# Kernel tuning notes

Measured on AMD Instinct MI355X. Metric: run time of the kernel, lower is better.

Reference implementation:

```python
import math
import jax, jax.numpy as jnp
import numpy as np

N_HEADS = 16

def setup_inputs() -> dict:
    key = jax.random.key(0)
    k1, k2, k3 = jax.random.split(key, 3)
    B, T, C = 2, 2048, 1024
    x = jax.random.normal(k1, (B, T, C), dtype=jnp.float32)
    # Linear weights stored as [in, out] so y = x @ W + b (same math as torch Linear)
    w_qkv = jax.random.normal(k2, (C, 3 * C), dtype=jnp.float32) * (1.0 / math.sqrt(C))
    b_qkv = jnp.zeros((3 * C,), dtype=jnp.float32)
    w_out = jax.random.normal(k3, (C, C), dtype=jnp.float32) * (1.0 / math.sqrt(C))
    b_out = jnp.zeros((C,), dtype=jnp.float32)
    return {"x": x, "w_qkv": w_qkv, "b_qkv": b_qkv, "w_out": w_out, "b_out": b_out}

def reference(x, w_qkv, b_qkv, w_out, b_out):
    B, T, C = x.shape
    H = N_HEADS
    hd = C // H
    qkv = (x @ w_qkv + b_qkv).reshape(B, T, 3, H, hd)
    q, k, v = qkv[:, :, 0], qkv[:, :, 1], qkv[:, :, 2]  # [B,T,H,hd]
    scale = 1.0 / math.sqrt(hd)
    att = jnp.einsum('bqhd,bkhd->bhqk', q, k) * scale  # [B,H,T,T]
    causal = jnp.tril(jnp.ones((T, T), dtype=bool))
    att = jnp.where(causal[None, None], att, jnp.float32(-jnp.inf))
    att = jax.nn.softmax(att, axis=-1)
    # dropout p=0.0 -> identity (eval mode)
    y = jnp.einsum('bhqk,bkhd->bqhd', att, v).reshape(B, T, C)
    return y @ w_out + b_out
```

## Files before the change

kernel.cpp:

```cpp
#include <hip/hip_runtime.h>
#include <hip/hip_bf16.h>
#include <stdint.h>


typedef __bf16 bf16_t;
typedef __attribute__((ext_vector_type(8))) __bf16 bf16x8;
typedef __attribute__((ext_vector_type(4))) __bf16 bf16x4;
typedef __attribute__((ext_vector_type(4))) short short4v;
typedef __attribute__((ext_vector_type(4))) float f32x4;

static_assert(sizeof(bf16x8) == 16, "bf16x8 must be 16B");

#if defined(__has_builtin)
#if __has_builtin(__builtin_amdgcn_mfma_f32_16x16x16bf16_1k)
#define HAVE_MFMA16 1
#endif
#if __has_builtin(__builtin_amdgcn_exp2f)
#define EXP2F(x) __builtin_amdgcn_exp2f(x)
#endif
#endif
#ifndef HAVE_MFMA16
#define HAVE_MFMA16 0
#endif
#ifndef EXP2F
#define EXP2F(x) exp2f(x)
#endif

__device__ inline void async_copy16(const bf16_t* gsrc, bf16_t* lds_dst) {
  __builtin_amdgcn_global_load_lds(
      (const __attribute__((address_space(1))) uint32_t*)(const void*)gsrc,
      (__attribute__((address_space(3))) uint32_t*)(void*)lds_dst,
      16, 0, 0);
}

__global__ __launch_bounds__(256) void prep_kernel(
    const float* __restrict__ x, const float* __restrict__ wq,
    const float* __restrict__ wo, bf16_t* __restrict__ xb,
    bf16_t* __restrict__ wqkvT, bf16_t* __restrict__ woutT) {
  __shared__ bf16_t tile[32][33];
  const int bid = blockIdx.x;
  if (bid < 2048) {
    const int i = bid * 256 + threadIdx.x;
    const float4* s = (const float4*)x;
    float4 a = s[i * 2], b = s[i * 2 + 1];
    bf16x8 o;
    o[0] = (bf16_t)a.x; o[1] = (bf16_t)a.y; o[2] = (bf16_t)a.z; o[3] = (bf16_t)a.w;
    o[4] = (bf16_t)b.x; o[5] = (bf16_t)b.y; o[6] = (bf16_t)b.z; o[7] = (bf16_t)b.w;
    ((bf16x8*)xb)[i] = o;
    return;
  }
  const bool isq = bid < 5120;
  const int id = isq ? bid - 2048 : bid - 5120;
  const int C = isq ? 3072 : 1024;
  const int R = 1024;
  const int nbx = isq ? 96 : 32;
  const float* in = isq ? wq : wo;
  bf16_t* out = isq ? wqkvT : woutT;
  const int c0 = (id % nbx) * 32, r0 = (id / nbx) * 32;
  const int tx = threadIdx.x & 31;
  const int ty = threadIdx.x >> 5;
#pragma unroll
  for (int i = 0; i < 4; i++) {
    int r = ty + i * 8;
    tile[r][tx] = (bf16_t)in[(size_t)(r0 + r) * C + c0 + tx];
  }
  __syncthreads();
#pragma unroll
  for (int i = 0; i < 4; i++) {
    int r = ty + i * 8;
    out[(size_t)(c0 + r) * R + r0 + tx] = tile[tx][r];
  }
}

template <bool OUT_F32>
__global__ __launch_bounds__(256) void gemm_bt_kernel(
    const bf16_t* __restrict__ A, const bf16_t* __restrict__ Bt,
    const float* __restrict__ bias, void* __restrict__ Cv, int M, int N,
    int K) {
  __shared__ __align__(16) bf16_t sA[128 * 32];
  __shared__ __align__(16) bf16_t sB[128 * 32];
  const int tid = threadIdx.x;
  const int wave = tid >> 6, lane = tid & 63;
  const int quad = lane >> 4, l16 = lane & 15;
  const int wm = (wave >> 1) * 64, wn = (wave & 1) * 64;
  const int bm = blockIdx.y * 128, bn = blockIdx.x * 128;

  const int srow = wave * 16 + (lane >> 2);
  const int skk = (lane & 3) * 8;
  const bf16_t* gA = A + (size_t)(bm + srow) * K + skk;
  const bf16_t* gB = Bt + (size_t)(bn + srow) * K + skk;
  bf16_t* lA = sA + wave * 512;
  bf16_t* lB = sB + wave * 512;

  f32x4 acc[4][4] = {};

  for (int k0 = 0; k0 < K; k0 += 32) {
    __syncthreads();
    async_copy16(gA + k0, lA);
    async_copy16(gA + (size_t)64 * K + k0, lA + 2048);
    async_copy16(gB + k0, lB);
    async_copy16(gB + (size_t)64 * K + k0, lB + 2048);
    __syncthreads();

    bf16x8 af[4], bfr[4];
#pragma unroll
    for (int i = 0; i < 4; i++)
      af[i] = *(const bf16x8*)&sA[(wm + i * 16 + l16) * 32 + quad * 8];
#pragma unroll
    for (int j = 0; j < 4; j++)
      bfr[j] = *(const bf16x8*)&sB[(wn + j * 16 + l16) * 32 + quad * 8];
#pragma unroll
    for (int i = 0; i < 4; i++)
#pragma unroll
      for (int j = 0; j < 4; j++)
        acc[i][j] = __builtin_amdgcn_mfma_f32_16x16x32_bf16(af[i], bfr[j],
                                                            acc[i][j], 0, 0, 0);
  }

#pragma unroll
  for (int j = 0; j < 4; j++) {
    const int col = bn + wn + j * 16 + l16;
    const float bv = bias[col];
#pragma unroll
    for (int i = 0; i < 4; i++) {
#pragma unroll
      for (int r = 0; r < 4; r++) {
        const int row = bm + wm + i * 16 + quad * 4 + r;
        const float v = acc[i][j][r] + bv;
        if (OUT_F32)
          ((float*)Cv)[(size_t)row * N + col] = v;
        else
          ((bf16_t*)Cv)[(size_t)row * N + col] = (bf16_t)v;
      }
    }
  }
}

#if HAVE_MFMA16
__global__ __launch_bounds__(256, 4) void attn_kernel(
    const bf16_t* __restrict__ qkv, bf16_t* __restrict__ Y) {
  constexpr int T = 2048, C3 = 3072;
  constexpr float CSC = 0.18033688f;
  constexpr float MB = 20.0f;
  __shared__ __align__(16) bf16_t sK[2][64 * 64];
  __shared__ __align__(16) bf16_t sVt[2][64 * 64];

  const int tid = threadIdx.x;
  const int wave = tid >> 6, lane = tid & 63;
  const int quad = lane >> 4, l16 = lane & 15;
  const int bh = blockIdx.y;
  const int flip = (bh >> 3) & 1;
  const int vv = ((int)blockIdx.x + ((bh >> 4) & 1) * 8) & 31;
  const int X = flip ? (31 - vv) : vv;
  const int q0 = X * 64;
  const int b = bh >> 4, h = bh & 15;
  const size_t base = (size_t)b * T * C3 + (size_t)h * 64;

  const int qrow = q0 + wave * 16 + l16;
  const bf16x8 qf0 = *(const bf16x8*)&qkv[base + (size_t)qrow * C3 + quad * 8];
  const bf16x8 qf1 =
      *(const bf16x8*)&qkv[base + (size_t)qrow * C3 + 32 + quad * 8];

  f32x4 o[4] = {};
  float l_acc = 0.f;

  const int t = tid >> 2, seg = tid & 3;
  const bf16_t* gK = &qkv[base + (size_t)t * C3 + 1024 + seg * 16];
  const int kq = tid >> 4, dq = tid & 15;
  const bf16_t* gV = &qkv[base + (size_t)(4 * kq) * C3 + 2048 + dq * 4];

  const int ktiles = X + 1;

  bf16x8 kr0 = *(const bf16x8*)gK;
  bf16x8 kr1 = *(const bf16x8*)(gK + 8);
  bf16x4 vA0 = *(const bf16x4*)gV;
  bf16x4 vA1 = *(const bf16x4*)(gV + C3);
  bf16x4 vA2 = *(const bf16x4*)(gV + 2 * C3);
  bf16x4 vA3 = *(const bf16x4*)(gV + 3 * C3);

  for (int kt = 0; kt < ktiles; kt++) {
    const int p = kt & 1;
    *(bf16x8*)&sK[p][t * 64 + (((2 * seg + 0) ^ (t & 7)) << 3)] = kr0;
    *(bf16x8*)&sK[p][t * 64 + (((2 * seg + 1) ^ (t & 7)) << 3)] = kr1;
#pragma unroll
    for (int i = 0; i < 4; i++) {
      const int d = dq * 4 + i;
      bf16x4 w;
      w[0] = vA0[i]; w[1] = vA1[i]; w[2] = vA2[i]; w[3] = vA3[i];
      *(bf16x4*)&sVt[p][d * 64 + ((kq ^ (d & 15)) << 2)] = w;
    }
    if (kt + 1 < ktiles) {
      const size_t off = (size_t)(kt + 1) * 64 * C3;
      kr0 = *(const bf16x8*)(gK + off);
      kr1 = *(const bf16x8*)(gK + off + 8);
      vA0 = *(const bf16x4*)(gV + off);
      vA1 = *(const bf16x4*)(gV + off + C3);
      vA2 = *(const bf16x4*)(gV + off + 2 * C3);
      vA3 = *(const bf16x4*)(gV + off + 3 * C3);
    }
    __syncthreads();

    const bool last = (kt == ktiles - 1);
    const int jmax = last ? wave : 3;
#pragma unroll
    for (int j = 0; j < 4; j++) {
      if (j > jmax) continue;
      const int trow = j * 16 + l16;
      bf16x8 kf0 = *(const bf16x8*)&sK[p][trow * 64 + ((quad ^ (trow & 7)) << 3)];
      bf16x8 kf1 =
          *(const bf16x8*)&sK[p][trow * 64 + (((4 + quad) ^ (trow & 7)) << 3)];
      f32x4 s2 = {};
      __builtin_amdgcn_s_setprio(1);
      s2 = __builtin_amdgcn_mfma_f32_16x16x32_bf16(kf0, qf0, s2, 0, 0, 0);
      s2 = __builtin_amdgcn_mfma_f32_16x16x32_bf16(kf1, qf1, s2, 0, 0, 0);
      __builtin_amdgcn_s_setprio(0);
      const bool diag = last && (j == wave);
#pragma unroll
      for (int r = 0; r < 4; r++) {
        float pv = EXP2F(fmaf(s2[r], CSC, -MB));
        if (diag && (quad * 4 + r > l16)) pv = 0.f;
        s2[r] = pv;
        l_acc += pv;
      }
      bf16x4 pb;
      pb[0] = (bf16_t)s2[0]; pb[1] = (bf16_t)s2[1];
      pb[2] = (bf16_t)s2[2]; pb[3] = (bf16_t)s2[3];
      union { bf16x4 b; short4v s; } u;
      u.b = pb;
      const short4v pa = u.s;
      __builtin_amdgcn_s_setprio(1);
#pragma unroll
      for (int n16 = 0; n16 < 4; n16++) {
        const int d = n16 * 16 + l16;
        const short4v vf = *(const short4v*)&sVt[p][d * 64 +
                                                    (((j * 4 + quad) ^ (d & 15))
                                                     << 2)];
        o[n16] =
            __builtin_amdgcn_mfma_f32_16x16x16bf16_1k(pa, vf, o[n16], 0, 0, 0);
      }
      __builtin_amdgcn_s_setprio(0);
    }
  }

  l_acc += __shfl_xor(l_acc, 16);
  l_acc += __shfl_xor(l_acc, 32);
#pragma unroll
  for (int r = 0; r < 4; r++) {
    const float lr = __shfl(l_acc, quad * 4 + r);
    const float inv = 1.0f / lr;
    const int row = q0 + wave * 16 + quad * 4 + r;
#pragma unroll
    for (int n16 = 0; n16 < 4; n16++)
      Y[((size_t)b * T + row) * 1024 + h * 64 + n16 * 16 + l16] =
          (bf16_t)(o[n16][r] * inv);
  }
}
#else
__global__ __launch_bounds__(256, 4) void attn_kernel(
    const bf16_t* __restrict__ qkv, bf16_t* __restrict__ Y) {
  constexpr int T = 2048, C3 = 3072;
  constexpr float CSC = 0.18033688f;
  constexpr float MB = 20.0f;
  __shared__ __align__(16) bf16_t sK[64 * 64];
  __shared__ __align__(16) bf16_t sVt[64 * 64];
  __shared__ __align__(16) bf16_t sP[4][16 * 64];

  const int tid = threadIdx.x;
  const int wave = tid >> 6, lane = tid & 63;
  const int quad = lane >> 4, l16 = lane & 15;
  const int bh = blockIdx.y;
  const int flip = (bh >> 3) & 1;
  const int vv = ((int)blockIdx.x + ((bh >> 4) & 1) * 8) & 31;
  const int X = flip ? (31 - vv) : vv;
  const int q0 = X * 64;
  const int b = bh >> 4, h = bh & 15;
  const size_t base = (size_t)b * T * C3 + (size_t)h * 64;

  const int qrow = q0 + wave * 16 + l16;
  const bf16x8 qf0 = *(const bf16x8*)&qkv[base + (size_t)qrow * C3 + quad * 8];
  const bf16x8 qf1 =
      *(const bf16x8*)&qkv[base + (size_t)qrow * C3 + 32 + quad * 8];

  f32x4 o[4] = {};
  float l_i[4] = {0.f, 0.f, 0.f, 0.f};

  const int t = tid >> 2, seg = tid & 3;
  const int tk = t & 7, tg3 = t >> 3;
  const bf16_t* gK = &qkv[base + (size_t)t * C3 + 1024 + seg * 16];
  const bf16_t* gV = &qkv[base + (size_t)t * C3 + 2048 + seg * 16];

  const int ktiles = X + 1;

  bf16x8 kr0 = *(const bf16x8*)gK;
  bf16x8 kr1 = *(const bf16x8*)(gK + 8);
  bf16x8 vr0 = *(const bf16x8*)gV;
  bf16x8 vr1 = *(const bf16x8*)(gV + 8);

  for (int kt = 0; kt < ktiles; kt++) {
    __syncthreads();
    *(bf16x8*)&sK[t * 64 + (((2 * seg + 0) ^ tk) << 3)] = kr0;
    *(bf16x8*)&sK[t * 64 + (((2 * seg + 1) ^ tk) << 3)] = kr1;
#pragma unroll
    for (int i = 0; i < 8; i++) {
      const int d = seg * 16 + i;
      sVt[d * 64 + ((tg3 ^ (d >> 3)) << 3) + (t & 7)] = vr0[i];
    }
#pragma unroll
    for (int i = 0; i < 8; i++) {
      const int d = seg * 16 + 8 + i;
      sVt[d * 64 + ((tg3 ^ (d >> 3)) << 3) + (t & 7)] = vr1[i];
    }
    __syncthreads();

    if (kt + 1 < ktiles) {
      const size_t off = (size_t)(kt + 1) * 64 * C3;
      kr0 = *(const bf16x8*)(gK + off);
      kr1 = *(const bf16x8*)(gK + off + 8);
      vr0 = *(const bf16x8*)(gV + off);
      vr1 = *(const bf16x8*)(gV + off + 8);
    }

    f32x4 s[4] = {};
#pragma unroll
    for (int j = 0; j < 4; j++) {
      const int kkey = l16 & 7;
      bf16x8 kf0 =
          *(const bf16x8*)&sK[(j * 16 + l16) * 64 + ((quad ^ kkey) << 3)];
      bf16x8 kf1 =
          *(const bf16x8*)&sK[(j * 16 + l16) * 64 + (((4 + quad) ^ kkey) << 3)];
      s[j] = __builtin_amdgcn_mfma_f32_16x16x32_bf16(qf0, kf0, s[j], 0, 0, 0);
      s[j] = __builtin_amdgcn_mfma_f32_16x16x32_bf16(qf1, kf1, s[j], 0, 0, 0);
    }

#pragma unroll
    for (int j = 0; j < 4; j++)
#pragma unroll
      for (int r = 0; r < 4; r++) s[j][r] = EXP2F(fmaf(s[j][r], CSC, -MB));
    if (kt == ktiles - 1) {
      const int k0 = kt * 64;
#pragma unroll
      for (int j = 0; j < 4; j++) {
        const int kcol = k0 + j * 16 + l16;
#pragma unroll
        for (int r = 0; r < 4; r++)
          if (kcol > q0 + wave * 16 + quad * 4 + r) s[j][r] = 0.f;
      }
    }
#pragma unroll
    for (int j = 0; j < 4; j++)
#pragma unroll
      for (int r = 0; r < 4; r++) l_i[r] += s[j][r];

    bf16_t* sp = &sP[wave][0];
#pragma unroll
    for (int j = 0; j < 4; j++)
#pragma unroll
      for (int r = 0; r < 4; r++) {
        const int m = quad * 4 + r;
        const int kw = (m + (m >> 3)) & 7;
        sp[m * 64 + ((((2 * j + (l16 >> 3)) ^ kw)) << 3) + (l16 & 7)] =
            (bf16_t)s[j][r];
      }

    const int kap = (l16 + (l16 >> 3)) & 7;
#pragma unroll
    for (int s2 = 0; s2 < 2; s2++) {
      bf16x8 pf =
          *(const bf16x8*)&sp[l16 * 64 + (((4 * s2 + quad) ^ kap) << 3)];
#pragma unroll
      for (int j = 0; j < 4; j++) {
        const int d = j * 16 + l16;
        bf16x8 vf =
            *(const bf16x8*)&sVt[d * 64 + (((4 * s2 + quad) ^ (d >> 3)) << 3)];
        o[j] = __builtin_amdgcn_mfma_f32_16x16x32_bf16(pf, vf, o[j], 0, 0, 0);
      }
    }
  }

#pragma unroll
  for (int r = 0; r < 4; r++) {
    float l = l_i[r];
#pragma unroll
    for (int off = 1; off < 16; off <<= 1) l += __shfl_xor(l, off);
    const float inv = 1.0f / l;
    const int row = q0 + wave * 16 + quad * 4 + r;
#pragma unroll
    for (int j = 0; j < 4; j++)
      Y[((size_t)b * T + row) * 1024 + h * 64 + j * 16 + l16] =
          (bf16_t)(o[j][r] * inv);
  }
}
#endif

extern "C" void kernel_launch(void* const* d_in, const int* in_sizes, int n_in,
                              void* d_out, int out_size, void* d_ws,
                              size_t ws_size, hipStream_t stream) {
  const float* x = nullptr;
  const float* w_qkv = nullptr;
  const float* b_qkv = nullptr;
  const float* w_out = nullptr;
  const float* b_out = nullptr;
  for (int i = 0; i < n_in; i++) {
    switch (in_sizes[i]) {
      case 4194304: x = (const float*)d_in[i]; break;
      case 3145728: w_qkv = (const float*)d_in[i]; break;
      case 3072:    b_qkv = (const float*)d_in[i]; break;
      case 1048576: w_out = (const float*)d_in[i]; break;
      case 1024:    b_out = (const float*)d_in[i]; break;
      default: break;
    }
  }
  float* out = (float*)d_out;

  bf16_t* xb = (bf16_t*)d_ws;
  bf16_t* wqkvT = xb + (size_t)4194304;
  bf16_t* woutT = wqkvT + (size_t)3145728;
  bf16_t* qkv = woutT + (size_t)1048576;
  bf16_t* Y = qkv + (size_t)12582912;

  prep_kernel<<<6144, 256, 0, stream>>>(x, w_qkv, w_out, xb, wqkvT, woutT);
  gemm_bt_kernel<false><<<dim3(24, 32), 256, 0, stream>>>(
      xb, wqkvT, b_qkv, (void*)qkv, 4096, 3072, 1024);
  attn_kernel<<<dim3(32, 32), 256, 0, stream>>>(qkv, Y);
  gemm_bt_kernel<true><<<dim3(8, 32), 256, 0, stream>>>(
      Y, woutT, b_out, (void*)out, 4096, 1024, 1024);
}
```

Before: 190.8 us.

## Pair causal query tiles per attention block for balanced work

Each attention block now processes two query tiles, X and 31-X, one after the other, so every block does the same total number of key tiles. The grid is halved to 16x32 blocks. This replaces the previous flip/rotate scheduling heuristic and aims to remove tail imbalance from the triangular causal workload. In exchange there are fewer blocks (512) to fill the GPU, and the two halves of each block run serially, with the first K/V tile of the second pass prefetched during the last iteration of the first.

New measurement: 195.5 us. 1.03x slower.

```diff
diff --git a/kernel.cpp b/kernel.cpp
--- a/kernel.cpp
+++ b/kernel.cpp
@@ -149,27 +149,13 @@
   const int wave = tid >> 6, lane = tid & 63;
   const int quad = lane >> 4, l16 = lane & 15;
   const int bh = blockIdx.y;
-  const int flip = (bh >> 3) & 1;
-  const int vv = ((int)blockIdx.x + ((bh >> 4) & 1) * 8) & 31;
-  const int X = flip ? (31 - vv) : vv;
-  const int q0 = X * 64;
   const int b = bh >> 4, h = bh & 15;
   const size_t base = (size_t)b * T * C3 + (size_t)h * 64;
-
-  const int qrow = q0 + wave * 16 + l16;
-  const bf16x8 qf0 = *(const bf16x8*)&qkv[base + (size_t)qrow * C3 + quad * 8];
-  const bf16x8 qf1 =
-      *(const bf16x8*)&qkv[base + (size_t)qrow * C3 + 32 + quad * 8];
-
-  f32x4 o[4] = {};
-  float l_acc = 0.f;
 
   const int t = tid >> 2, seg = tid & 3;
   const bf16_t* gK = &qkv[base + (size_t)t * C3 + 1024 + seg * 16];
   const int kq = tid >> 4, dq = tid & 15;
   const bf16_t* gV = &qkv[base + (size_t)(4 * kq) * C3 + 2048 + dq * 4];
-
-  const int ktiles = X + 1;
 
   bf16x8 kr0 = *(const bf16x8*)gK;
   bf16x8 kr1 = *(const bf16x8*)(gK + 8);
@@ -178,81 +164,101 @@
   bf16x4 vA2 = *(const bf16x4*)(gV + 2 * C3);
   bf16x4 vA3 = *(const bf16x4*)(gV + 3 * C3);
 
-  for (int kt = 0; kt < ktiles; kt++) {
-    const int p = kt & 1;
-    *(bf16x8*)&sK[p][t * 64 + (((2 * seg + 0) ^ (t & 7)) << 3)] = kr0;
-    *(bf16x8*)&sK[p][t * 64 + (((2 * seg + 1) ^ (t & 7)) << 3)] = kr1;
-#pragma unroll
-    for (int i = 0; i < 4; i++) {
-      const int d = dq * 4 + i;
-      bf16x4 w;
-      w[0] = vA0[i]; w[1] = vA1[i]; w[2] = vA2[i]; w[3] = vA3[i];
-      *(bf16x4*)&sVt[p][d * 64 + ((kq ^ (d & 15)) << 2)] = w;
-    }
-    if (kt + 1 < ktiles) {
-      const size_t off = (size_t)(kt + 1) * 64 * C3;
-      kr0 = *(const bf16x8*)(gK + off);
-      kr1 = *(const bf16x8*)(gK + off + 8);
-      vA0 = *(const bf16x4*)(gV + off);
-      vA1 = *(const bf16x4*)(gV + off + C3);
-      vA2 = *(const bf16x4*)(gV + off + 2 * C3);
-      vA3 = *(const bf16x4*)(gV + off + 3 * C3);
-    }
-    __syncthreads();
-
-    const bool last = (kt == ktiles - 1);
-    const int jmax = last ? wave : 3;
-#pragma unroll
-    for (int j = 0; j < 4; j++) {
-      if (j > jmax) continue;
-      const int trow = j * 16 + l16;
-      bf16x8 kf0 = *(const bf16x8*)&sK[p][trow * 64 + ((quad ^ (trow & 7)) << 3)];
-      bf16x8 kf1 =
-          *(const bf16x8*)&sK[p][trow * 64 + (((4 + quad) ^ (trow & 7)) << 3)];
-      f32x4 s2 = {};
-      __builtin_amdgcn_s_setprio(1);
-      s2 = __builtin_amdgcn_mfma_f32_16x16x32_bf16(kf0, qf0, s2, 0, 0, 0);
-      s2 = __builtin_amdgcn_mfma_f32_16x16x32_bf16(kf1, qf1, s2, 0, 0, 0);
-      __builtin_amdgcn_s_setprio(0);
-      const bool diag = last && (j == wave);
-#pragma unroll
-      for (int r = 0; r < 4; r++) {
-        float pv = EXP2F(fmaf(s2[r], CSC, -MB));
-        if (diag && (quad * 4 + r > l16)) pv = 0.f;
-        s2[r] = pv;
-        l_acc += pv;
-      }
-      bf16x4 pb;
-      pb[0] = (bf16_t)s2[0]; pb[1] = (bf16_t)s2[1];
-      pb[2] = (bf16_t)s2[2]; pb[3] = (bf16_t)s2[3];
-      union { bf16x4 b; short4v s; } u;
-      u.b = pb;
-      const short4v pa = u.s;
-      __builtin_amdgcn_s_setprio(1);
-#pragma unroll
-      for (int n16 = 0; n16 < 4; n16++) {
-        const int d = n16 * 16 + l16;
-        const short4v vf = *(const short4v*)&sVt[p][d * 64 +
-                                                    (((j * 4 + quad) ^ (d & 15))
-                                                     << 2)];
-        o[n16] =
-            __builtin_amdgcn_mfma_f32_16x16x16bf16_1k(pa, vf, o[n16], 0, 0, 0);
-      }
-      __builtin_amdgcn_s_setprio(0);
-    }
-  }
-
-  l_acc += __shfl_xor(l_acc, 16);
-  l_acc += __shfl_xor(l_acc, 32);
-#pragma unroll
-  for (int r = 0; r < 4; r++) {
-    const float lr = __shfl(l_acc, quad * 4 + r);
-    const float inv = 1.0f / lr;
-    const int row = q0 + wave * 16 + quad * 4 + r;
-#pragma unroll
-    for (int n16 = 0; n16 < 4; n16++)
-      Y[((size_t)b * T + row) * 1024 + h * 64 + n16 * 16 + l16] =
-          (bf16_t)(o[n16][r] * inv);
+#pragma unroll 1
+  for (int qs = 0; qs < 2; qs++) {
+    const int X = qs ? (31 - (int)blockIdx.x) : (int)blockIdx.x;
+    const int q0 = X * 64;
+    const int qrow = q0 + wave * 16 + l16;
+    const bf16x8 qf0 =
+        *(const bf16x8*)&qkv[base + (size_t)qrow * C3 + quad * 8];
+    const bf16x8 qf1 =
+        *(const bf16x8*)&qkv[base + (size_t)qrow * C3 + 32 + quad * 8];
+
+    f32x4 o[4] = {};
+    float l_acc = 0.f;
+    const int ktiles = X + 1;
+
+    if (qs) __syncthreads();
+
+    for (int kt = 0; kt < ktiles; kt++) {
+      const int p = kt & 1;
+      *(bf16x8*)&sK[p][t * 64 + (((2 * seg + 0) ^ (t & 7)) << 3)] = kr0;
+      *(bf16x8*)&sK[p][t * 64 + (((2 * seg + 1) ^ (t & 7)) << 3)] = kr1;
+#pragma unroll
+      for (int i = 0; i < 4; i++) {
+        const int d = dq * 4 + i;
+        bf16x4 w;
+        w[0] = vA0[i]; w[1] = vA1[i]; w[2] = vA2[i]; w[3] = vA3[i];
+        *(bf16x4*)&sVt[p][d * 64 + ((kq ^ (d & 15)) << 2)] = w;
+      }
+      const int nkt = (kt + 1 < ktiles) ? (kt + 1) : (qs ? -1 : 0);
+      if (nkt >= 0) {
+        const size_t off = (size_t)nkt * 64 * C3;
+        kr0 = *(const bf16x8*)(gK + off);
+        kr1 = *(const bf16x8*)(gK + off + 8);
+        vA0 = *(const bf16x4*)(gV + off);
+        vA1 = *(const bf16x4*)(gV + off + C3);
+        vA2 = *(const bf16x4*)(gV + off + 2 * C3);
+        vA3 = *(const bf16x4*)(gV + off + 3 * C3);
+      }
+      __syncthreads();
+
+      const bool last = (kt == ktiles - 1);
+      const int jmax = last ? wave : 3;
+#pragma unroll
+      for (int j = 0; j < 4; j++) {
+        if (j > jmax) continue;
+        const int trow = j * 16 + l16;
+        bf16x8 kf0 =
+            *(const bf16x8*)&sK[p][trow * 64 + ((quad ^ (trow & 7)) << 3)];
+        bf16x8 kf1 =
+            *(const bf16x8*)&sK[p][trow * 64 + (((4 + quad) ^ (trow & 7)) << 3)];
+        f32x4 s2 = {};
+        __builtin_amdgcn_s_setprio(1);
+        s2 = __builtin_amdgcn_mfma_f32_16x16x32_bf16(kf0, qf0, s2, 0, 0, 0);
+        s2 = __builtin_amdgcn_mfma_f32_16x16x32_bf16(kf1, qf1, s2, 0, 0, 0);
+        __builtin_amdgcn_s_setprio(0);
+        const bool diag = last && (j == wave);
+#pragma unroll
+        for (int r = 0; r < 4; r++) {
+          float pv = EXP2F(fmaf(s2[r], CSC, -MB));
+          if (diag && (quad * 4 + r > l16)) pv = 0.f;
+          s2[r] = pv;
+          l_acc += pv;
+        }
+        bf16x4 pb;
+        pb[0] = (bf16_t)s2[0]; pb[1] = (bf16_t)s2[1];
+        pb[2] = (bf16_t)s2[2]; pb[3] = (bf16_t)s2[3];
+        union { bf16x4 bv; short4v sv; } u;
+        u.bv = pb;
+        const short4v pa = u.sv;
+        __builtin_amdgcn_s_setprio(1);
+#pragma unroll
+        for (int n16 = 0; n16 < 4; n16++) {
+          const int d = n16 * 16 + l16;
+          const short4v vf = *(const short4v*)&sVt[p][d * 64 +
+                                                      (((j * 4 + quad) ^
+                                                        (d & 15))
+                                                       << 2)];
+          o[n16] = __builtin_amdgcn_mfma_f32_16x16x16bf16_1k(pa, vf, o[n16],
+                                                             0, 0, 0);
+        }
+        __builtin_amdgcn_s_setprio(0);
+      }
+    }
+
+    l_acc += __shfl_xor(l_acc, 16);
+    l_acc += __shfl_xor(l_acc, 32);
+#pragma unroll
+    for (int r = 0; r < 4; r++) {
+      const float lr = __shfl(l_acc, quad * 4 + r);
+      const float inv = 1.0f / lr;
+      const int row = q0 + wave * 16 + quad * 4 + r;
+#pragma unroll
+      for (int n16 = 0; n16 < 4; n16++)
+        Y[((size_t)b * T + row) * 1024 + h * 64 + n16 * 16 + l16] =
+            (bf16_t)(o[n16][r] * inv);
+    }
   }
 }
 #else
@@ -269,125 +275,128 @@
   const int wave = tid >> 6, lane = tid & 63;
   const int quad = lane >> 4, l16 = lane & 15;
   const int bh = blockIdx.y;
-  const int flip = (bh >> 3) & 1;
-  const int vv = ((int)blockIdx.x + ((bh >> 4) & 1) * 8) & 31;
-  const int X = flip ? (31 - vv) : vv;
-  const int q0 = X * 64;
   const int b = bh >> 4, h = bh & 15;
   const size_t base = (size_t)b * T * C3 + (size_t)h * 64;
-
-  const int qrow = q0 + wave * 16 + l16;
-  const bf16x8 qf0 = *(const bf16x8*)&qkv[base + (size_t)qrow * C3 + quad * 8];
-  const bf16x8 qf1 =
-      *(const bf16x8*)&qkv[base + (size_t)qrow * C3 + 32 + quad * 8];
-
-  f32x4 o[4] = {};
-  float l_i[4] = {0.f, 0.f, 0.f, 0.f};
 
   const int t = tid >> 2, seg = tid & 3;
   const int tk = t & 7, tg3 = t >> 3;
   const bf16_t* gK = &qkv[base + (size_t)t * C3 + 1024 + seg * 16];
   const bf16_t* gV = &qkv[base + (size_t)t * C3 + 2048 + seg * 16];
 
-  const int ktiles = X + 1;
-
-  bf16x8 kr0 = *(const bf16x8*)gK;
-  bf16x8 kr1 = *(const bf16x8*)(gK + 8);
-  bf16x8 vr0 = *(const bf16x8*)gV;
-  bf16x8 vr1 = *(const bf16x8*)(gV + 8);
-
-  for (int kt = 0; kt < ktiles; kt++) {
-    __syncthreads();
-    *(bf16x8*)&sK[t * 64 + (((2 * seg + 0) ^ tk) << 3)] = kr0;
-    *(bf16x8*)&sK[t * 64 + (((2 * seg + 1) ^ tk) << 3)] = kr1;
-#pragma unroll
-    for (int i = 0; i < 8; i++) {
-      const int d = seg * 16 + i;
-      sVt[d * 64 + ((tg3 ^ (d >> 3)) << 3) + (t & 7)] = vr0[i];
-    }
-#pragma unroll
-    for (int i = 0; i < 8; i++) {
-      const int d = seg * 16 + 8 + i;
-      sVt[d * 64 + ((tg3 ^ (d >> 3)) << 3) + (t & 7)] = vr1[i];
-    }
-    __syncthreads();
-
-    if (kt + 1 < ktiles) {
-      const size_t off = (size_t)(kt + 1) * 64 * C3;
-      kr0 = *(const bf16x8*)(gK + off);
-      kr1 = *(const bf16x8*)(gK + off + 8);
-      vr0 = *(const bf16x8*)(gV + off);
-      vr1 = *(const bf16x8*)(gV + off + 8);
-    }
-
-    f32x4 s[4] = {};
-#pragma unroll
-    for (int j = 0; j < 4; j++) {
-      const int kkey = l16 & 7;
-      bf16x8 kf0 =
-          *(const bf16x8*)&sK[(j * 16 + l16) * 64 + ((quad ^ kkey) << 3)];
-      bf16x8 kf1 =
-          *(const bf16x8*)&sK[(j * 16 + l16) * 64 + (((4 + quad) ^ kkey) << 3)];
-      s[j] = __builtin_amdgcn_mfma_f32_16x16x32_bf16(qf0, kf0, s[j], 0, 0, 0);
-      s[j] = __builtin_amdgcn_mfma_f32_16x16x32_bf16(qf1, kf1, s[j], 0, 0, 0);
-    }
-
-#pragma unroll
-    for (int j = 0; j < 4; j++)
-#pragma unroll
-      for (int r = 0; r < 4; r++) s[j][r] = EXP2F(fmaf(s[j][r], CSC, -MB));
-    if (kt == ktiles - 1) {
-      const int k0 = kt * 64;
+#pragma unroll 1
+  for (int qs = 0; qs < 2; qs++) {
+    const int X = qs ? (31 - (int)blockIdx.x) : (int)blockIdx.x;
+    const int q0 = X * 64;
+    const int qrow = q0 + wave * 16 + l16;
+    const bf16x8 qf0 =
+        *(const bf16x8*)&qkv[base + (size_t)qrow * C3 + quad * 8];
+    const bf16x8 qf1 =
+        *(const bf16x8*)&qkv[base + (size_t)qrow * C3 + 32 + quad * 8];
+
+    f32x4 o[4] = {};
+    float l_i[4] = {0.f, 0.f, 0.f, 0.f};
+    const int ktiles = X + 1;
+
+    bf16x8 kr0 = *(const bf16x8*)gK;
+    bf16x8 kr1 = *(const bf16x8*)(gK + 8);
+    bf16x8 vr0 = *(const bf16x8*)gV;
+    bf16x8 vr1 = *(const bf16x8*)(gV + 8);
+
+    for (int kt = 0; kt < ktiles; kt++) {
+      __syncthreads();
+      *(bf16x8*)&sK[t * 64 + (((2 * seg + 0) ^ tk) << 3)] = kr0;
+      *(bf16x8*)&sK[t * 64 + (((2 * seg + 1) ^ tk) << 3)] = kr1;
+#pragma unroll
+      for (int i = 0; i < 8; i++) {
+        const int d = seg * 16 + i;
+        sVt[d * 64 + ((tg3 ^ (d >> 3)) << 3) + (t & 7)] = vr0[i];
+      }
+#pragma unroll
+      for (int i = 0; i < 8; i++) {
+        const int d = seg * 16 + 8 + i;
+        sVt[d * 64 + ((tg3 ^ (d >> 3)) << 3) + (t & 7)] = vr1[i];
+      }
+      __syncthreads();
+
+      if (kt + 1 < ktiles) {
+        const size_t off = (size_t)(kt + 1) * 64 * C3;
+        kr0 = *(const bf16x8*)(gK + off);
+        kr1 = *(const bf16x8*)(gK + off + 8);
+        vr0 = *(const bf16x8*)(gV + off);
+        vr1 = *(const bf16x8*)(gV + off + 8);
+      }
+
+      f32x4 s[4] = {};
 #pragma unroll
       for (int j = 0; j < 4; j++) {
-        const int kcol = k0 + j * 16 + l16;
-#pragma unroll
-        for (int r = 0; r < 4; r++)
-          if (kcol > q0 + wave * 16 + quad * 4 + r) s[j][r] = 0.f;
-      }
-    }
-#pragma unroll
-    for (int j = 0; j < 4; j++)
-#pragma unroll
-      for (int r = 0; r < 4; r++) l_i[r] += s[j][r];
-
-    bf16_t* sp = &sP[wave][0];
-#pragma unroll
-    for (int j = 0; j < 4; j++)
-#pragma unroll
-      for (int r = 0; r < 4; r++) {
-        const int m = quad * 4 + r;
-        const int kw = (m + (m >> 3)) & 7;
-        sp[m * 64 + ((((2 * j + (l16 >> 3)) ^ kw)) << 3) + (l16 & 7)] =
-            (bf16_t)s[j][r];
-      }
-
-    const int kap = (l16 + (l16 >> 3)) & 7;
-#pragma unroll
-    for (int s2 = 0; s2 < 2; s2++) {
-      bf16x8 pf =
-          *(const bf16x8*)&sp[l16 * 64 + (((4 * s2 + quad) ^ kap) << 3)];
-#pragma unroll
-      for (int j = 0; j < 4; j++) {
-        const int d = j * 16 + l16;
-        bf16x8 vf =
-            *(const bf16x8*)&sVt[d * 64 + (((4 * s2 + quad) ^ (d >> 3)) << 3)];
-        o[j] = __builtin_amdgcn_mfma_f32_16x16x32_bf16(pf, vf, o[j], 0, 0, 0);
-      }
-    }
-  }
-
-#pragma unroll
-  for (int r = 0; r < 4; r++) {
-    float l = l_i[r];
-#pragma unroll
-    for (int off = 1; off < 16; off <<= 1) l += __shfl_xor(l, off);
-    const float inv = 1.0f / l;
-    const int row = q0 + wave * 16 + quad * 4 + r;
-#pragma unroll
-    for (int j = 0; j < 4; j++)
-      Y[((size_t)b * T + row) * 1024 + h * 64 + j * 16 + l16] =
-          (bf16_t)(o[j][r] * inv);
+        const int kkey = l16 & 7;
+        bf16x8 kf0 =
+            *(const bf16x8*)&sK[(j * 16 + l16) * 64 + ((quad ^ kkey) << 3)];
+        bf16x8 kf1 =
+            *(const bf16x8*)&sK[(j * 16 + l16) * 64 +
+                                (((4 + quad) ^ kkey) << 3)];
+        s[j] = __builtin_amdgcn_mfma_f32_16x16x32_bf16(qf0, kf0, s[j], 0, 0, 0);
+        s[j] = __builtin_amdgcn_mfma_f32_16x16x32_bf16(qf1, kf1, s[j], 0, 0, 0);
+      }
+
+#pragma unroll
+      for (int j = 0; j < 4; j++)
+#pragma unroll
+        for (int r = 0; r < 4; r++) s[j][r] = EXP2F(fmaf(s[j][r], CSC, -MB));
+      if (kt == ktiles - 1) {
+        const int k0 = kt * 64;
+#pragma unroll
+        for (int j = 0; j < 4; j++) {
+          const int kcol = k0 + j * 16 + l16;
+#pragma unroll
+          for (int r = 0; r < 4; r++)
+            if (kcol > q0 + wave * 16 + quad * 4 + r) s[j][r] = 0.f;
+        }
+      }
+#pragma unroll
+      for (int j = 0; j < 4; j++)
+#pragma unroll
+        for (int r = 0; r < 4; r++) l_i[r] += s[j][r];
+
+      bf16_t* sp = &sP[wave][0];
+#pragma unroll
+      for (int j = 0; j < 4; j++)
+#pragma unroll
+        for (int r = 0; r < 4; r++) {
+          const int m = quad * 4 + r;
+          const int kw = (m + (m >> 3)) & 7;
+          sp[m * 64 + ((((2 * j + (l16 >> 3)) ^ kw)) << 3) + (l16 & 7)] =
+              (bf16_t)s[j][r];
+        }
+
+      const int kap = (l16 + (l16 >> 3)) & 7;
+#pragma unroll
+      for (int s2 = 0; s2 < 2; s2++) {
+        bf16x8 pf =
+            *(const bf16x8*)&sp[l16 * 64 + (((4 * s2 + quad) ^ kap) << 3)];
+#pragma unroll
+        for (int j = 0; j < 4; j++) {
+          const int d = j * 16 + l16;
+          bf16x8 vf =
+              *(const bf16x8*)&sVt[d * 64 +
+                                   (((4 * s2 + quad) ^ (d >> 3)) << 3)];
+          o[j] = __builtin_amdgcn_mfma_f32_16x16x32_bf16(pf, vf, o[j], 0, 0, 0);
+        }
+      }
+    }
+
+#pragma unroll
+    for (int r = 0; r < 4; r++) {
+      float l = l_i[r];
+#pragma unroll
+      for (int off = 1; off < 16; off <<= 1) l += __shfl_xor(l, off);
+      const float inv = 1.0f / l;
+      const int row = q0 + wave * 16 + quad * 4 + r;
+#pragma unroll
+      for (int j = 0; j < 4; j++)
+        Y[((size_t)b * T + row) * 1024 + h * 64 + j * 16 + l16] =
+            (bf16_t)(o[j][r] * inv);
+    }
   }
 }
 #endif
@@ -421,7 +430,7 @@
   prep_kernel<<<6144, 256, 0, stream>>>(x, w_qkv, w_out, xb, wqkvT, woutT);
   gemm_bt_kernel<false><<<dim3(24, 32), 256, 0, stream>>>(
       xb, wqkvT, b_qkv, (void*)qkv, 4096, 3072, 1024);
-  attn_kernel<<<dim3(32, 32), 256, 0, stream>>>(qkv, Y);
+  attn_kernel<<<dim3(16, 32), 256, 0, stream>>>(qkv, Y);
   gemm_bt_kernel<true><<<dim3(8, 32), 256, 0, stream>>>(
       Y, woutT, b_out, (void*)out, 4096, 1024, 1024);
 }
```
